# Optimization experiments

Hardware: AMD Instinct MI355X
Metric: run time of the kernel (lower is better)

## Reference

```python
import jax, jax.numpy as jnp
import numpy as np

B, C, H, W = 8, 256, 128, 128
WH, WW = 8, 8
M, NH = 4, 8
N = WH * WW
HD = C // NH
SCALE = HD ** -0.5


def _ln(x, g, b, eps=1e-5):
    m = x.mean(-1, keepdims=True)
    v = ((x - m) ** 2).mean(-1, keepdims=True)
    return (x - m) / jnp.sqrt(v + eps) * g + b


def _wpart(x):
    # (B, H, W, C) -> (B*nW, WH*WW, C)
    b, h, w, c = x.shape
    x = x.reshape(b, h // WH, WH, w // WW, WW, c).transpose(0, 1, 3, 2, 4, 5)
    return x.reshape(-1, N, c)


def _wrev(x, h, w):
    # (B*nW, WH*WW, C) -> (B, H, W, C)
    c = x.shape[-1]
    b = x.shape[0] // ((h // WH) * (w // WW))
    x = x.reshape(b, h // WH, w // WW, WH, WW, c).transpose(0, 1, 3, 2, 4, 5)
    return x.reshape(b, h, w, c)


def setup_inputs() -> dict:
    key = jax.random.key(0)
    ks = iter(jax.random.split(key, 16))

    def rn(shape, s=0.02):
        return jax.random.normal(next(ks), shape, jnp.float32) * s

    z = lambda *s: jnp.zeros(s, jnp.float32)
    o = lambda *s: jnp.ones(s, jnp.float32)
    return {
        'F_R': jax.random.normal(next(ks), (B, C, H, W), jnp.float32),
        'F_T': jax.random.normal(next(ks), (B, C, H, W), jnp.float32),
        'r_R': jax.random.uniform(next(ks), (B, 1, H, W), jnp.float32),
        'r_T': jax.random.uniform(next(ks), (B, 1, H, W), jnp.float32),
        'psi_w': rn((2 * C, M)), 'psi_b': z(M),
        'phi_w': rn((2 * C, 2 * C)), 'phi_b': z(2 * C),
        'np_g': o(2 * C), 'np_b': z(2 * C),
        'nz_g': o(C), 'nz_b': z(C),
        'rpb_table': rn(((2 * WH - 1) * (2 * WW - 1), NH)),
        'q_w': rn((C, C)), 'q_b': z(C),
        'k_w': rn((C, C)), 'k_b': z(C),
        'v_w': rn((C, C)), 'v_b': z(C),
        'nzf_g': o(C), 'nzf_b': z(C),
        'fc1_w': rn((C, 4 * C)), 'fc1_b': z(4 * C),
        'fc2_w': rn((4 * C, C)), 'fc2_b': z(C),
        'nr_g': o(C), 'nr_b': z(C),
        'nt_g': o(C), 'nt_b': z(C),
        'g1_w': rn((2, 8)), 'g1_b': z(8),
        'g2_w': rn((8, 1)), 'g2_b': z(1),
    }


def reference(F_R, F_T, r_R, r_T, psi_w, psi_b, phi_w, phi_b, np_g, np_b,
              nz_g, nz_b, rpb_table, q_w, q_b, k_w, k_b, v_w, v_b,
              nzf_g, nzf_b, fc1_w, fc1_b, fc2_w, fc2_b, nr_g, nr_b,
              nt_g, nt_b, g1_w, g1_b, g2_w, g2_b):
    # NOTE: rpb_table corresponds to relative_position_bias_table; the original
    # forward computes attn_mask = rel_pos_bias + local_mask but never applies it
    # (dead code), so it does not affect the output.
    FRw = _wpart(jnp.transpose(F_R, (0, 2, 3, 1)))  # (Bn, N, C)
    FTw = _wpart(jnp.transpose(F_T, (0, 2, 3, 1)))

    # attention pooling to mediators
    F_hat = _ln(jnp.concatenate([FRw, FTw], axis=-1), np_g, np_b)  # (Bn, N, 2C)
    A_m = jax.nn.softmax(F_hat @ psi_w + psi_b, axis=1)            # (Bn, N, M)
    Z = jnp.einsum('bnm,bnd->bmd', A_m, F_hat @ phi_w + phi_b)     # (Bn, M, 2C)
    Z = _ln((Z[..., :C] + Z[..., C:]) * 0.5, nz_g, nz_b)           # (Bn, M, C)

    rRw = _wpart(jnp.transpose(r_R, (0, 2, 3, 1)))[..., 0]  # (Bn, N)
    rTw = _wpart(jnp.transpose(r_T, (0, 2, 3, 1)))[..., 0]

    # mediators attend to each windowed stream
    QZ = (Z @ q_w + q_b).reshape(-1, M, NH, HD)
    KR = (FRw @ k_w + k_b).reshape(-1, N, NH, HD)
    VR = (FRw @ v_w + v_b).reshape(-1, N, NH, HD)
    KT = (FTw @ k_w + k_b).reshape(-1, N, NH, HD)
    VT = (FTw @ v_w + v_b).reshape(-1, N, NH, HD)

    aR = jax.nn.softmax(jnp.einsum('bmhd,bnhd->bhmn', QZ, KR) * SCALE
                        * rRw[:, None, None, :], axis=-1)
    ZhR = jnp.einsum('bhmn,bnhd->bmhd', aR, VR).reshape(-1, M, C)
    aT = jax.nn.softmax(jnp.einsum('bmhd,bnhd->bhmn', QZ, KT) * SCALE
                        * rTw[:, None, None, :], axis=-1)
    ZhT = jnp.einsum('bhmn,bnhd->bmhd', aT, VT).reshape(-1, M, C)

    Zp = _ln(Z + ZhR + ZhT, nzf_g, nzf_b)
    Zp = jax.nn.gelu(Zp @ fc1_w + fc1_b, approximate=False) @ fc2_w + fc2_b

    # windows attend back to mediators (note cross r usage, as in the original)
    QR = (FRw @ q_w + q_b).reshape(-1, N, NH, HD)
    QT = (FTw @ q_w + q_b).reshape(-1, N, NH, HD)
    KZ = (Zp @ k_w + k_b).reshape(-1, M, NH, HD)
    VZ = (Zp @ v_w + v_b).reshape(-1, M, NH, HD)

    aZR = jax.nn.softmax(jnp.einsum('bnhd,bmhd->bhnm', QR, KZ) * SCALE
                         * rTw[:, None, :, None], axis=-1)
    FRh = jnp.einsum('bhnm,bmhd->bnhd', aZR, VZ).reshape(-1, N, C)
    aZT = jax.nn.softmax(jnp.einsum('bnhd,bmhd->bhnm', QT, KZ) * SCALE
                         * rRw[:, None, :, None], axis=-1)
    FTh = jnp.einsum('bhnm,bmhd->bnhd', aZT, VZ).reshape(-1, N, C)

    FRp = jnp.transpose(_wrev(_ln(FRw + FRh, nr_g, nr_b), H, W), (0, 3, 1, 2))
    FTp = jnp.transpose(_wrev(_ln(FTw + FTh, nt_g, nt_b), H, W), (0, 3, 1, 2))

    # gating from globally pooled relevance maps
    g_in = jnp.concatenate([r_R.mean((2, 3)), r_T.mean((2, 3))], axis=1)  # (B,2)
    gamma = jax.nn.sigmoid(jax.nn.relu(g_in @ g1_w + g1_b) @ g2_w + g2_b)  # (B,1)
    gamma = gamma[:, :, None, None]
    return gamma * FRp + (1.0 - gamma) * FTp
```

## Files before the change

kernel.cpp:

```cpp
#include <hip/hip_runtime.h>
#include <math.h>

#define SCALE 0.17677669529663687f

#define OFF_FRW  0l
#define OFF_FTW  33554432l
#define OFF_RRW  67108864l
#define OFF_RTW  67239936l
#define OFF_G    67371008l
#define OFF_Z    71565312l
#define OFF_ZP   73662464l
#define OFF_ZP2  75759616l
#define OFF_QT   77856768l
#define OFF_KT   77922304l
#define OFF_VT   77987840l
#define OFF_F1T  78053376l
#define OFF_PHIT 78315520l
#define OFF_PHB  78446592l
#define OFF_GAM  78446848l

__device__ __forceinline__ float wsum64(float v){
  #pragma unroll
  for(int o=32;o>0;o>>=1) v+=__shfl_xor(v,o,64);
  return v;
}
__device__ __forceinline__ float wmax64(float v){
  #pragma unroll
  for(int o=32;o>0;o>>=1) v=fmaxf(v,__shfl_xor(v,o,64));
  return v;
}
__device__ __forceinline__ float blockSum256(float v, float* red, int t){
  v=wsum64(v);
  __syncthreads();
  if((t&63)==0) red[t>>6]=v;
  __syncthreads();
  return red[0]+red[1]+red[2]+red[3];
}

__global__ __launch_bounds__(256) void k_prep(const float* __restrict__ qw, const float* __restrict__ kw,
                       const float* __restrict__ vw, const float* __restrict__ fc1w,
                       const float* __restrict__ phiw, const float* __restrict__ phibv,
                       float* __restrict__ ws){
  long gid = (long)blockIdx.x*256 + threadIdx.x;
  if(gid < 262144){ long o=gid>>8, i=gid&255; ws[OFF_F1T+gid] = fc1w[i*1024+o]; return; }
  gid -= 262144;
  if(gid < 65536){ long o=gid>>8, i=gid&255; ws[OFF_QT+gid] = qw[i*256+o]; return; }
  gid -= 65536;
  if(gid < 65536){ long o=gid>>8, i=gid&255; ws[OFF_KT+gid] = kw[i*256+o]; return; }
  gid -= 65536;
  if(gid < 65536){ long o=gid>>8, i=gid&255; ws[OFF_VT+gid] = vw[i*256+o]; return; }
  gid -= 65536;
  if(gid < 131072){ long c=gid>>9, k=gid&511; ws[OFF_PHIT+gid] = 0.5f*(phiw[k*512+c] + phiw[k*512+c+256]); return; }
  gid -= 131072;
  if(gid < 256){ ws[OFF_PHB+gid] = 0.5f*(phibv[gid] + phibv[gid+256]); }
}

__global__ __launch_bounds__(256) void k_gamma(const float* __restrict__ rR, const float* __restrict__ rT,
                        const float* __restrict__ g1w, const float* __restrict__ g1b,
                        const float* __restrict__ g2w, const float* __restrict__ g2b,
                        float* __restrict__ ws){
// ... 40 lines not shown
    }
    __syncthreads();
    int cl=t&31, tg=t>>5;
    for(int tok=tg; tok<1024; tok+=8){
      int wc=tok>>6, n=tok&63, i=n>>3, j=n&7;
      float v = tile[cl*TSTRC + i*TSTRI + wc*8+j];
      long w = ((long)b*16+wr)*16+wc;
      dst[(w*64+n)*256 + cchunk*32 + cl] = v;
    }
  }
  if(cchunk==0){
    for(int q=0;q<2;q++){
      const float* src=q? rT:rR;
      float* dst=ws + (q? OFF_RTW:OFF_RRW);
      for(int tok=t; tok<1024; tok+=256){
        int wc=tok>>6, n=tok&63, i=n>>3, j=n&7;
        long w=((long)b*16+wr)*16+wc;
        dst[w*64+n] = src[((long)b*128 + wr*8+i)*128 + wc*8+j];
      }
    }
  }
}

#define FS 516
__global__ __launch_bounds__(512) void k_stage1(const float* __restrict__ psiw, const float* __restrict__ psib,
                         const float* __restrict__ npg, const float* __restrict__ npb,
                         float* __restrict__ ws){
  __shared__ float F[64*FS];
  __shared__ float psiT[2048];
  __shared__ float ng[512], nb[512];
  __shared__ float mu[64], rsd[64];
  __shared__ float Sp[2048];
  __shared__ float Sa[256];
  int w=blockIdx.x, t=threadIdx.x;
  const float* FRw = ws+OFF_FRW + (long)w*16384;
  const float* FTw = ws+OFF_FTW + (long)w*16384;
  for(int i4=t;i4<8192;i4+=512){
    int n=i4>>7, cq=i4&127; int c=cq*4;
    float4 v = (c<256)? *(const float4*)(FRw + n*256+c) : *(const float4*)(FTw + n*256+c-256);
    float* p=&F[n*FS+c]; p[0]=v.x; p[1]=v.y; p[2]=v.z; p[3]=v.w;
  }
  ng[t&511]=npg[t&511]; nb[t&511]=npb[t&511];
  for(int i=t;i<2048;i+=512){ int c=i>>2, m=i&3; psiT[m*512+c]=psiw[i]; }
  __syncthreads();
  { int g=t>>6, l=t&63;
    for(int n=g;n<64;n+=8){
      float s1=0.f,s2=0.f;
      #pragma unroll
      for(int k=0;k<8;k++){ float x=F[n*FS + l + 64*k]; s1+=x; s2+=x*x; }
      s1=wsum64(s1); s2=wsum64(s2);
      if(l==0){ float mm=s1*(1.f/512.f), vv=s2*(1.f/512.f)-mm*mm; mu[n]=mm; rsd[n]=rsqrtf(vv+1e-5f); }
    } }
  __syncthreads();
  for(int i=t;i<32768;i+=512){ int n=i>>9, c=i&511; F[n*FS+c] = (F[n*FS+c]-mu[n])*rsd[n]*ng[c]+nb[c]; }
  __syncthreads();
  { int n=t&63, sl=t>>6; int c0=sl*64;
    float a0=0.f,a1=0.f,a2=0.f,a3=0.f;
    for(int k=0;k<64;k+=4){
      int c=c0+k;
      float4 f=*(const float4*)&F[n*FS+c];
      float4 p0=*(const float4*)&psiT[c];
      float4 p1=*(const float4*)&psiT[512+c];
      float4 p2=*(const float4*)&psiT[1024+c];
      float4 p3=*(const float4*)&psiT[1536+c];
      a0+=f.x*p0.x+f.y*p0.y+f.z*p0.z+f.w*p0.w;
      a1+=f.x*p1.x+f.y*p1.y+f.z*p1.z+f.w*p1.w;
      a2+=f.x*p2.x+f.y*p2.y+f.z*p2.z+f.w*p2.w;
      a3+=f.x*p3.x+f.y*p3.y+f.z*p3.z+f.w*p3.w;
    }
    float4 sv; sv.x=a0; sv.y=a1; sv.z=a2; sv.w=a3;
    *(float4*)&Sp[(sl*64+n)*4]=sv;
  }
  __syncthreads();
  if(t<256){ int n=t>>2, m=t&3;
    float s=psib[m];
    for(int sl=0;sl<8;sl++) s+=Sp[(sl*64+n)*4+m];
    Sa[n*4+m]=s;
  }
  __syncthreads();
  if(t<64){
    #pragma unroll
    for(int m=0;m<4;m++){
      float v=Sa[t*4+m];
      float mx=wmax64(v);
      float e=expf(v-mx);
      float sm=wsum64(e);
      Sa[t*4+m]=e/sm;
    } }
  __syncthreads();
  { int c=t;
    float a0=0.f,a1=0.f,a2=0.f,a3=0.f;
    for(int n=0;n<64;n++){
      float f=F[n*FS+c];
      float4 am=*(const float4*)&Sa[n*4];
      a0+=am.x*f; a1+=am.y*f; a2+=am.z*f; a3+=am.w*f;
    }
    float* G=ws+OFF_G+(long)w*2048;
    G[c]=a0; G[512+c]=a1; G[1024+c]=a2; G[1536+c]=a3;
  }
}

__global__ __launch_bounds__(256) void k_z(const float* __restrict__ nzg, const float* __restrict__ nzb,
                    float* __restrict__ ws){
  __shared__ float Gw[2048];
  __shared__ float red[4];
  int w=blockIdx.x, t=threadIdx.x;
  const float* G=ws+OFF_G+(long)w*2048;
  for(int i4=t;i4<512;i4+=256){ *(float4*)&Gw[i4*4] = *(const float4*)&G[i4*4]; }
  __syncthreads();
  const float* phiT=ws+OFF_PHIT;
  const float* phb=ws+OFF_PHB;
  int c=t;
  float pb=phb[c];
  float a0=pb,a1=pb,a2=pb,a3=pb;
  const float* prow = phiT + (long)c*512;
  for(int k=0;k<512;k+=4){
// ... 1 lines not shown
    float4 g0=*(const float4*)&Gw[k];
    float4 g1=*(const float4*)&Gw[512+k];
    float4 g2=*(const float4*)&Gw[1024+k];
    float4 g3=*(const float4*)&Gw[1536+k];
    a0+=g0.x*pv.x+g0.y*pv.y+g0.z*pv.z+g0.w*pv.w;
    a1+=g1.x*pv.x+g1.y*pv.y+g1.z*pv.z+g1.w*pv.w;
    a2+=g2.x*pv.x+g2.y*pv.y+g2.z*pv.z+g2.w*pv.w;
    a3+=g3.x*pv.x+g3.y*pv.y+g3.z*pv.z+g3.w*pv.w;
  }
  float* Z=ws+OFF_Z+(long)w*1024;
  float g=nzg[c], b=nzb[c];
  float vals[4]={a0,a1,a2,a3};
  #pragma unroll
  for(int m=0;m<4;m++){
    float v=vals[m];
    float s1=blockSum256(v,red,t);
    float s2=blockSum256(v*v,red,t);
    float mm=s1*(1.f/256.f), vv=s2*(1.f/256.f)-mm*mm;
    float rs=rsqrtf(vv+1e-5f);
    Z[m*256+c]=(v-mm)*rs*g+b;
  }
}

#define FLS 260
__global__ __launch_bounds__(256) void k_attn1(const float* __restrict__ qb, const float* __restrict__ kw,
    const float* __restrict__ kb, const float* __restrict__ vb,
    const float* __restrict__ nzfg, const float* __restrict__ nzfb,
    float* __restrict__ ws){
  __shared__ float Fl[64*FLS];
  __shared__ float Qp[8192];
  __shared__ float Wl[8192];
  __shared__ float Zl[1024];
  __shared__ float QZ[1024];
  __shared__ float Al[2048];
  __shared__ float cbs[32];
  __shared__ float rl[64];
  __shared__ float red[4];
  int w=blockIdx.x, t=threadIdx.x;
  {
    const float* Z=ws+OFF_Z+(long)w*1024;
    for(int i=t;i<1024;i+=256) Zl[i]=Z[i];
  }
  __syncthreads();
  {
    const float* qrow=ws+OFF_QT+(long)t*256;
    float b0=qb[t];
    float a0=b0,a1=b0,a2=b0,a3=b0;
    for(int k=0;k<256;k+=4){
      float4 q4=*(const float4*)(qrow+k);
      float4 z0=*(const float4*)&Zl[k];
      float4 z1=*(const float4*)&Zl[256+k];
      float4 z2=*(const float4*)&Zl[512+k];
      float4 z3=*(const float4*)&Zl[768+k];
      a0+=z0.x*q4.x+z0.y*q4.y+z0.z*q4.z+z0.w*q4.w;
      a1+=z1.x*q4.x+z1.y*q4.y+z1.z*q4.z+z1.w*q4.w;
      a2+=z2.x*q4.x+z2.y*q4.y+z2.z*q4.z+z2.w*q4.w;
      a3+=z3.x*q4.x+z3.y*q4.y+z3.z*q4.z+z3.w*q4.w;
    }
    QZ[t]=a0; QZ[256+t]=a1; QZ[512+t]=a2; QZ[768+t]=a3;
  }
  __syncthreads();
  {
    const float* krow=kw+(long)t*256;
    for(int h=0;h<8;h++){
      float a0=0.f,a1=0.f,a2=0.f,a3=0.f;
      for(int d=0;d<32;d+=4){
        float4 k4=*(const float4*)(krow+h*32+d);
        float4 q0=*(const float4*)&QZ[h*32+d];
        float4 q1=*(const float4*)&QZ[256+h*32+d];
        float4 q2=*(const float4*)&QZ[512+h*32+d];
        float4 q3=*(const float4*)&QZ[768+h*32+d];
        a0+=k4.x*q0.x+k4.y*q0.y+k4.z*q0.z+k4.w*q0.w;
        a1+=k4.x*q1.x+k4.y*q1.y+k4.z*q1.z+k4.w*q1.w;
        a2+=k4.x*q2.x+k4.y*q2.y+k4.z*q2.z+k4.w*q2.w;
        a3+=k4.x*q3.x+k4.y*q3.y+k4.z*q3.z+k4.w*q3.w;
      }
      Qp[(h*4+0)*256+t]=a0; Qp[(h*4+1)*256+t]=a1; Qp[(h*4+2)*256+t]=a2; Qp[(h*4+3)*256+t]=a3;
    }
  }
  if(t<32){ int h=t>>2, m=t&3;
    float a=0.f;
    for(int d=0;d<32;d++) a+=kb[h*32+d]*QZ[m*256+h*32+d];
    cbs[t]=a;
  }
  for(int s=0;s<2;s++){
    __syncthreads();
    const float* Fsrc=ws+(s?OFF_FTW:OFF_FRW)+(long)w*16384;
    const float* rsrc=ws+(s?OFF_RTW:OFF_RRW)+(long)w*64;
    for(int i4=t;i4<4096;i4+=256){
      int n=i4>>6, cq=i4&63;
      float4 v=*(const float4*)(Fsrc+n*256+cq*4);
      float* p=&Fl[n*FLS+cq*4];
      p[0]=v.x; p[1]=v.y; p[2]=v.z; p[3]=v.w;
    }
    if(t<64) rl[t]=rsrc[t];
    __syncthreads();
    {
      int n=t&63, g=t>>6;
      const float* frow=&Fl[n*FLS];
      float acc[8];
      #pragma unroll
      for(int q=0;q<8;q++) acc[q]=cbs[q*4+g];
      for(int k=0;k<256;k+=4){
        float4 f=*(const float4*)(frow+k);
        #pragma unroll
        for(int q=0;q<8;q++){
          float4 p=*(const float4*)&Qp[(q*4+g)*256+k];
          acc[q]+=f.x*p.x+f.y*p.y+f.z*p.z+f.w*p.w;
        }
      }
      float sr=SCALE*rl[n];
      #pragma unroll
      for(int q=0;q<8;q++){
        float a=acc[q]*sr;
        float mx=wmax64(a);
        float e=expf(a-mx);
        float sm=wsum64(e);
        Al[(q*4+g)*64+n]=e/sm;
      }
    }
    __syncthreads();
    {
      int c=t;
      float wacc[32];
      #pragma unroll
      for(int P=0;P<32;P++) wacc[P]=0.f;
      for(int n0=0;n0<64;n0+=4){
        float f0=Fl[(n0+0)*FLS+c], f1=Fl[(n0+1)*FLS+c], f2=Fl[(n0+2)*FLS+c], f3=Fl[(n0+3)*FLS+c];
        #pragma unroll
        for(int P=0;P<32;P++){
          float4 a4=*(const float4*)&Al[P*64+n0];
          wacc[P]+=a4.x*f0+a4.y*f1+a4.z*f2+a4.w*f3;
        }
      }
      if(s==0){
        #pragma unroll
        for(int P=0;P<32;P++) Wl[P*256+c]=wacc[P];
      }else{
        #pragma unroll
        for(int P=0;P<32;P++) Wl[P*256+c]+=wacc[P];
      }
    }
  }
  __syncthreads();
  float zh0,zh1,zh2,zh3;
  {
    int co=t, h=co>>5;
    const float* vrow=ws+OFF_VT+(long)co*256;
    float vb2=2.f*vb[co];
    float a0=vb2,a1=vb2,a2=vb2,a3=vb2;
    for(int k=0;k<256;k+=4){
      float4 v4=*(const float4*)(vrow+k);
      float4 w0=*(const float4*)&Wl[(h*4+0)*256+k];
      float4 w1=*(const float4*)&Wl[(h*4+1)*256+k];
      float4 w2=*(const float4*)&Wl[(h*4+2)*256+k];
      float4 w3=*(const float4*)&Wl[(h*4+3)*256+k];
      a0+=w0.x*v4.x+w0.y*v4.y+w0.z*v4.z+w0.w*v4.w;
      a1+=w1.x*v4.x+w1.y*v4.y+w1.z*v4.z+w1.w*v4.w;
      a2+=w2.x*v4.x+w2.y*v4.y+w2.z*v4.z+w2.w*v4.w;
      a3+=w3.x*v4.x+w3.y*v4.y+w3.z*v4.z+w3.w*v4.w;
    }
    zh0=a0; zh1=a1; zh2=a2; zh3=a3;
  }
  {
    int c=t;
    float g=nzfg[c], b=nzfb[c];
    float* Zp=ws+OFF_ZP+(long)w*1024;
    float v4[4]={Zl[c]+zh0, Zl[256+c]+zh1, Zl[512+c]+zh2, Zl[768+c]+zh3};
    #pragma unroll
    for(int m=0;m<4;m++){
      float v=v4[m];
      float s1=blockSum256(v,red,t);
      float s2=blockSum256(v*v,red,t);
      float mm=s1*(1.f/256.f), vv=s2*(1.f/256.f)-mm*mm;
      float rs=rsqrtf(vv+1e-5f);
      Zp[m*256+c]=(v-mm)*rs*g+b;
    }
  }
}

__global__ __launch_bounds__(256) void k_mlp(const float* __restrict__ fc1b, const float* __restrict__ fc2w,
                      const float* __restrict__ fc2b, float* __restrict__ ws){
  __shared__ float Zpl[8192];
  __shared__ float Hc[4096];
  int blk=blockIdx.x, t=threadIdx.x;
  long r0=(long)blk*32;
  const float* Zp=ws+OFF_ZP + r0*256;
  for(int i4=t;i4<2048;i4+=256){ *(float4*)&Zpl[i4*4] = *(const float4*)&Zp[i4*4]; }
  float o[32];
  { float b=fc2b[t];
    #pragma unroll
    for(int r=0;r<32;r++) o[r]=b; }
  const float* f1T=ws+OFF_F1T;
  for(int ch=0;ch<8;ch++){
    __syncthreads();
    { int jl=t&127, rg=t>>7;
      int j=ch*128+jl;
      const float* wrow=f1T+(long)j*256;
      float acc[16];
      #pragma unroll
      for(int i=0;i<16;i++) acc[i]=0.f;
      for(int k=0;k<256;k+=4){
        float4 w4=*(const float4*)(wrow+k);
        #pragma unroll
        for(int i=0;i<16;i++){
          float4 z=*(const float4*)&Zpl[(rg*16+i)*256+k];
          acc[i]+=z.x*w4.x+z.y*w4.y+z.z*w4.z+z.w*w4.w;
        }
      }
      float bj=fc1b[j];
      #pragma unroll
      for(int i=0;i<16;i++){
        float x=acc[i]+bj;
        Hc[(rg*16+i)*128+jl]=0.5f*x*(1.f+erff(x*0.70710678118654752f));
      }
    }
    __syncthreads();
    { int c=t;
      const float* f2=fc2w+(long)(ch*128)*256+c;
      for(int j=0;j<128;j++){
        float wv=f2[(long)j*256];
        #pragma unroll
        for(int r=0;r<32;r++) o[r]+=Hc[r*128+j]*wv;
      }
    }
  }
  __syncthreads();
  float* Zp2=ws+OFF_ZP2 + r0*256;
  #pragma unroll
  for(int r=0;r<32;r++) Zp2[(long)r*256+t]=o[r];
}

__global__ __launch_bounds__(256) void k_final(const float* __restrict__ kbv, const float* __restrict__ qw,
    const float* __restrict__ qbv, const float* __restrict__ vbv,
    const float* __restrict__ nrg, const float* __restrict__ nrb,
    const float* __restrict__ ntg, const float* __restrict__ ntb,
    float* __restrict__ out, float* __restrict__ ws){
  __shared__ float Fl[64*FLS];
  __shared__ float Kp[8192];
  __shared__ float Z2[1024];
  __shared__ float KZ[1024];
  __shared__ float VZ[1024];
  __shared__ float Al[2048];
  __shared__ float cb2[32];
  __shared__ float rl[64];
  int w=blockIdx.x, t=threadIdx.x;
  int b=w>>8, wr=(w>>4)&15, wc=w&15;
  {
    const float* Zp2=ws+OFF_ZP2+(long)w*1024;
    for(int i=t;i<1024;i+=256) Z2[i]=Zp2[i];
  }
  __syncthreads();
  {
    const float* krow=ws+OFF_KT+(long)t*256;
    const float* vrow=ws+OFF_VT+(long)t*256;
    float kb0=kbv[t], vb0=vbv[t];
    float k0=kb0,k1=kb0,k2=kb0,k3=kb0, v0=vb0,v1=vb0,v2=vb0,v3=vb0;
    for(int k=0;k<256;k+=4){
      float4 kk=*(const float4*)(krow+k);
      float4 vv=*(const float4*)(vrow+k);
      float4 z0=*(const float4*)&Z2[k];
      float4 z1=*(const float4*)&Z2[256+k];
      float4 z2=*(const float4*)&Z2[512+k];
      float4 z3=*(const float4*)&Z2[768+k];
      k0+=z0.x*kk.x+z0.y*kk.y+z0.z*kk.z+z0.w*kk.w;
      k1+=z1.x*kk.x+z1.y*kk.y+z1.z*kk.z+z1.w*kk.w;
      k2+=z2.x*kk.x+z2.y*kk.y+z2.z*kk.z+z2.w*kk.w;
      k3+=z3.x*kk.x+z3.y*kk.y+z3.z*kk.z+z3.w*kk.w;
      v0+=z0.x*vv.x+z0.y*vv.y+z0.z*vv.z+z0.w*vv.w;
      v1+=z1.x*vv.x+z1.y*vv.y+z1.z*vv.z+z1.w*vv.w;
      v2+=z2.x*vv.x+z2.y*vv.y+z2.z*vv.z+z2.w*vv.w;
      v3+=z3.x*vv.x+z3.y*vv.y+z3.z*vv.z+z3.w*vv.w;
    }
    KZ[t]=k0; KZ[256+t]=k1; KZ[512+t]=k2; KZ[768+t]=k3;
    VZ[t]=v0; VZ[256+t]=v1; VZ[512+t]=v2; VZ[768+t]=v3;
  }
  __syncthreads();
  {
    const float* qrow=qw+(long)t*256;
    for(int h=0;h<8;h++){
      float a0=0.f,a1=0.f,a2=0.f,a3=0.f;
      for(int d=0;d<32;d+=4){
        float4 q4=*(const float4*)(qrow+h*32+d);
        float4 c0=*(const float4*)&KZ[h*32+d];
        float4 c1=*(const float4*)&KZ[256+h*32+d];
        float4 c2=*(const float4*)&KZ[512+h*32+d];
        float4 c3=*(const float4*)&KZ[768+h*32+d];
        a0+=q4.x*c0.x+q4.y*c0.y+q4.z*c0.z+q4.w*c0.w;
        a1+=q4.x*c1.x+q4.y*c1.y+q4.z*c1.z+q4.w*c1.w;
        a2+=q4.x*c2.x+q4.y*c2.y+q4.z*c2.z+q4.w*c2.w;
        a3+=q4.x*c3.x+q4.y*c3.y+q4.z*c3.z+q4.w*c3.w;
      }
      Kp[(h*4+0)*256+t]=a0; Kp[(h*4+1)*256+t]=a1; Kp[(h*4+2)*256+t]=a2; Kp[(h*4+3)*256+t]=a3;
    }
  }
  if(t<32){ int h=t>>2, m=t&3;
    float a=0.f;
    for(int d=0;d<32;d++) a+=qbv[h*32+d]*KZ[m*256+h*32+d];
    cb2[t]=a;
  }
  float gam=ws[OFF_GAM+b];
  float oa[64];
  int lane=t&63, wv=t>>6;
  for(int s=0;s<2;s++){
    __syncthreads();
    const float* Fsrc=ws+(s?OFF_FTW:OFF_FRW)+(long)w*16384;
    const float* rsrc=ws+(s?OFF_RRW:OFF_RTW)+(long)w*64;
    for(int i4=t;i4<4096;i4+=256){
      int n=i4>>6, cq=i4&63;
      float4 v=*(const float4*)(Fsrc+n*256+cq*4);
      float* p=&Fl[n*FLS+cq*4];
      p[0]=v.x; p[1]=v.y; p[2]=v.z; p[3]=v.w;
    }
    if(t<64) rl[t]=rsrc[t];
    __syncthreads();
    {
      int n=lane;
      const float* frow=&Fl[n*FLS];
      float sr=SCALE*rl[n];
      #pragma unroll
      for(int hh=0;hh<2;hh++){
        int h=wv*2+hh;
        float a0=cb2[h*4+0],a1=cb2[h*4+1],a2=cb2[h*4+2],a3=cb2[h*4+3];
        for(int k=0;k<256;k+=4){
          float4 f=*(const float4*)(frow+k);
          float4 p0=*(const float4*)&Kp[(h*4+0)*256+k];
          float4 p1=*(const float4*)&Kp[(h*4+1)*256+k];
          float4 p2=*(const float4*)&Kp[(h*4+2)*256+k];
          float4 p3=*(const float4*)&Kp[(h*4+3)*256+k];
          a0+=f.x*p0.x+f.y*p0.y+f.z*p0.z+f.w*p0.w;
          a1+=f.x*p1.x+f.y*p1.y+f.z*p1.z+f.w*p1.w;
          a2+=f.x*p2.x+f.y*p2.y+f.z*p2.z+f.w*p2.w;
          a3+=f.x*p3.x+f.y*p3.y+f.z*p3.z+f.w*p3.w;
        }
        a0*=sr; a1*=sr; a2*=sr; a3*=sr;
        float mx=fmaxf(fmaxf(a0,a1),fmaxf(a2,a3));
        float e0=expf(a0-mx),e1=expf(a1-mx),e2=expf(a2-mx),e3=expf(a3-mx);
        float inv=1.f/(e0+e1+e2+e3);
        float4 av; av.x=e0*inv; av.y=e1*inv; av.z=e2*inv; av.w=e3*inv;
        *(float4*)&Al[(h*64+n)*4]=av;
      }
    }
    __syncthreads();
    {
      float gsc = s? (1.f-gam) : gam;
      float vzr[4][4], gA[4], bA[4];
      #pragma unroll
      for(int e=0;e<4;e++){
        int c=lane+64*e;
        #pragma unroll
        for(int m=0;m<4;m++) vzr[e][m]=VZ[m*256+c];
        gA[e]= s? ntg[c]:nrg[c];
        bA[e]= s? ntb[c]:nrb[c];
      }
      for(int k=0;k<16;k++){
        int n=wv+4*k;
        float val[4]; float s1=0.f,s2=0.f;
        #pragma unroll
        for(int e=0;e<4;e++){
          int c=lane+64*e; int h=c>>5;
          float4 a4=*(const float4*)&Al[(h*64+n)*4];
          float v=Fl[n*FLS+c] + a4.x*vzr[e][0]+a4.y*vzr[e][1]+a4.z*vzr[e][2]+a4.w*vzr[e][3];
          val[e]=v; s1+=v; s2+=v*v;
        }
        s1=wsum64(s1); s2=wsum64(s2);
        float mm=s1*(1.f/256.f), vv2=s2*(1.f/256.f)-mm*mm;
        float rs=rsqrtf(vv2+1e-5f);
        #pragma unroll
        for(int e=0;e<4;e++){
          float lnv=(val[e]-mm)*rs*gA[e]+bA[e];
          if(s==0) oa[k*4+e]=gsc*lnv; else oa[k*4+e]+=gsc*lnv;
        }
      }
    }
  }
  __syncthreads();
  for(int k=0;k<16;k++){
    int n=wv+4*k;
    #pragma unroll
    for(int e=0;e<4;e++){ Fl[n*FLS+lane+64*e]=oa[k*4+e]; }
  }
  __syncthreads();
  {
    int c=t;
    long obase=((long)b*256+c)*16384 + (long)wr*1024 + wc*8;
    for(int i=0;i<8;i++){
      float4 v0, v1;
      v0.x=Fl[(i*8+0)*FLS+c]; v0.y=Fl[(i*8+1)*FLS+c]; v0.z=Fl[(i*8+2)*FLS+c]; v0.w=Fl[(i*8+3)*FLS+c];
      v1.x=Fl[(i*8+4)*FLS+c]; v1.y=Fl[(i*8+5)*FLS+c]; v1.z=Fl[(i*8+6)*FLS+c]; v1.w=Fl[(i*8+7)*FLS+c];
      *(float4*)(out+obase+(long)i*128)=v0;
      *(float4*)(out+obase+(long)i*128+4)=v1;
    }
  }
}

extern "C" void kernel_launch(void* const* d_in, const int* in_sizes, int n_in,
                              void* d_out, int out_size, void* d_ws, size_t ws_size,
                              hipStream_t stream){
  (void)in_sizes; (void)n_in; (void)out_size; (void)ws_size;
  const float* F_R=(const float*)d_in[0];
  const float* F_T=(const float*)d_in[1];
  const float* r_R=(const float*)d_in[2];
  const float* r_T=(const float*)d_in[3];
  const float* psi_w=(const float*)d_in[4];
  const float* psi_b=(const float*)d_in[5];
  const float* phi_w=(const float*)d_in[6];
  const float* phi_b=(const float*)d_in[7];
  const float* np_g=(const float*)d_in[8];
  const float* np_b=(const float*)d_in[9];
  const float* nz_g=(const float*)d_in[10];
  const float* nz_b=(const float*)d_in[11];
  const float* q_w=(const float*)d_in[13];
// ... 4 lines not shown
  const float* v_b=(const float*)d_in[18];
  const float* nzf_g=(const float*)d_in[19];
  const float* nzf_b=(const float*)d_in[20];
  const float* fc1_w=(const float*)d_in[21];
  const float* fc1_b=(const float*)d_in[22];
  const float* fc2_w=(const float*)d_in[23];
  const float* fc2_b=(const float*)d_in[24];
  const float* nr_g=(const float*)d_in[25];
  const float* nr_b=(const float*)d_in[26];
  const float* nt_g=(const float*)d_in[27];
  const float* nt_b=(const float*)d_in[28];
  const float* g1_w=(const float*)d_in[29];
  const float* g1_b=(const float*)d_in[30];
  const float* g2_w=(const float*)d_in[31];
  const float* g2_b=(const float*)d_in[32];
  float* ws=(float*)d_ws;
  float* out=(float*)d_out;

  hipLaunchKernelGGL(k_prep,  dim3(2305), dim3(256), 0, stream, q_w,k_w,v_w,fc1_w,phi_w,phi_b,ws);
  hipLaunchKernelGGL(k_gamma, dim3(8),    dim3(256), 0, stream, r_R,r_T,g1_w,g1_b,g2_w,g2_b,ws);
  hipLaunchKernelGGL(k_win,   dim3(8,16,8), dim3(256), 0, stream, F_R,F_T,r_R,r_T,ws);
  hipLaunchKernelGGL(k_stage1,dim3(2048), dim3(512), 0, stream, psi_w,psi_b,np_g,np_b,ws);
  hipLaunchKernelGGL(k_z,     dim3(2048), dim3(256), 0, stream, nz_g,nz_b,ws);
  hipLaunchKernelGGL(k_attn1, dim3(2048), dim3(256), 0, stream, q_b,k_w,k_b,v_b,nzf_g,nzf_b,ws);
  hipLaunchKernelGGL(k_mlp,   dim3(256),  dim3(256), 0, stream, fc1_b,fc2_w,fc2_b,ws);
  hipLaunchKernelGGL(k_final, dim3(2048), dim3(256), 0, stream, k_b,q_w,q_b,v_b,nr_g,nr_b,nt_g,nt_b,out,ws);
}
```

Measured before the change: 2.428 ms.

## Swizzle shared-memory layouts and double threads per block in attention kernels

Replaces padded shared-memory rows with an XOR swizzle in stage1, attn1 and final so the row and column reads avoid bank conflicts without padding. The attn1 and final kernels move from 256 to 512 threads: matvec reductions are split into two K-halves and summed through shared memory, and the per-head score and output work is split across the extra waves. The MLP kernel processes 16 rows per block instead of 32, doubling its grid. This aims to raise occupancy and latency hiding, at the cost of extra barriers and partial-sum passes, plus higher register and LDS pressure per block.

```diff
diff --git a/kernel.cpp b/kernel.cpp
--- a/kernel.cpp
+++ b/kernel.cpp
@@ -36,6 +36,18 @@
   __syncthreads();
   return red[0]+red[1]+red[2]+red[3];
 }
+__device__ __forceinline__ float blockSum512(float v, float* red, int t){
+  v=wsum64(v);
+  __syncthreads();
+  if((t&63)==0) red[t>>6]=v;
+  __syncthreads();
+  return red[0]+red[1]+red[2]+red[3]+red[4]+red[5]+red[6]+red[7];
+}
+
+__device__ __forceinline__ int swz(int n, int c){ return (n<<8) + ((((c>>2)^(n&15))<<2) | (c&3)); }
+__device__ __forceinline__ int swz4(int n, int c4){ return (n<<8) + ((c4^(n&15))<<2); }
+__device__ __forceinline__ int swz512(int n, int c){ return (n<<9) + ((((c>>2)^(n&15))<<2) | (c&3)); }
+__device__ __forceinline__ int swz512_4(int n, int c4){ return (n<<9) + ((c4^(n&15))<<2); }
 
 __global__ __launch_bounds__(256) void k_prep(const float* __restrict__ qw, const float* __restrict__ kw,
                        const float* __restrict__ vw, const float* __restrict__ fc1w,
@@ -122,11 +134,10 @@
   }
 }
 
-#define FS 516
 __global__ __launch_bounds__(512) void k_stage1(const float* __restrict__ psiw, const float* __restrict__ psib,
                          const float* __restrict__ npg, const float* __restrict__ npb,
                          float* __restrict__ ws){
-  __shared__ float F[64*FS];
+  __shared__ float F[64*512];
   __shared__ float psiT[2048];
   __shared__ float ng[512], nb[512];
   __shared__ float mu[64], rsd[64];
@@ -138,27 +149,27 @@
   for(int i4=t;i4<8192;i4+=512){
     int n=i4>>7, cq=i4&127; int c=cq*4;
     float4 v = (c<256)? *(const float4*)(FRw + n*256+c) : *(const float4*)(FTw + n*256+c-256);
-    float* p=&F[n*FS+c]; p[0]=v.x; p[1]=v.y; p[2]=v.z; p[3]=v.w;
-  }
-  ng[t&511]=npg[t&511]; nb[t&511]=npb[t&511];
+    *(float4*)&F[swz512_4(n,cq)] = v;
+  }
+  ng[t]=npg[t]; nb[t]=npb[t];
   for(int i=t;i<2048;i+=512){ int c=i>>2, m=i&3; psiT[m*512+c]=psiw[i]; }
   __syncthreads();
   { int g=t>>6, l=t&63;
     for(int n=g;n<64;n+=8){
       float s1=0.f,s2=0.f;
       #pragma unroll
-      for(int k=0;k<8;k++){ float x=F[n*FS + l + 64*k]; s1+=x; s2+=x*x; }
+      for(int k=0;k<8;k++){ float x=F[swz512(n, l+64*k)]; s1+=x; s2+=x*x; }
       s1=wsum64(s1); s2=wsum64(s2);
       if(l==0){ float mm=s1*(1.f/512.f), vv=s2*(1.f/512.f)-mm*mm; mu[n]=mm; rsd[n]=rsqrtf(vv+1e-5f); }
     } }
   __syncthreads();
-  for(int i=t;i<32768;i+=512){ int n=i>>9, c=i&511; F[n*FS+c] = (F[n*FS+c]-mu[n])*rsd[n]*ng[c]+nb[c]; }
-  __syncthreads();
-  { int n=t&63, sl=t>>6; int c0=sl*64;
+  for(int i=t;i<32768;i+=512){ int n=i>>9, c=i&511; int a=swz512(n,c); F[a] = (F[a]-mu[n])*rsd[n]*ng[c]+nb[c]; }
+  __syncthreads();
+  { int n=t&63, sl=t>>6; int c0=sl*64; int nx=n&15;
     float a0=0.f,a1=0.f,a2=0.f,a3=0.f;
     for(int k=0;k<64;k+=4){
-      int c=c0+k;
-      float4 f=*(const float4*)&F[n*FS+c];
+      int c=c0+k; int c4=c>>2;
+      float4 f=*(const float4*)&F[swz512_4(n,c4)];
       float4 p0=*(const float4*)&psiT[c];
       float4 p1=*(const float4*)&psiT[512+c];
       float4 p2=*(const float4*)&psiT[1024+c];
@@ -170,6 +181,7 @@
     }
     float4 sv; sv.x=a0; sv.y=a1; sv.z=a2; sv.w=a3;
     *(float4*)&Sp[(sl*64+n)*4]=sv;
+    (void)nx;
   }
   __syncthreads();
   if(t<256){ int n=t>>2, m=t&3;
@@ -191,7 +203,7 @@
   { int c=t;
     float a0=0.f,a1=0.f,a2=0.f,a3=0.f;
     for(int n=0;n<64;n++){
-      float f=F[n*FS+c];
+      float f=F[swz512(n,c)];
       float4 am=*(const float4*)&Sa[n*4];
       a0+=am.x*f; a1+=am.y*f; a2+=am.z*f; a3+=am.w*f;
     }
@@ -239,12 +251,11 @@
   }
 }
 
-#define FLS 260
-__global__ __launch_bounds__(256) void k_attn1(const float* __restrict__ qb, const float* __restrict__ kw,
+__global__ __launch_bounds__(512) void k_attn1(const float* __restrict__ qb, const float* __restrict__ kw,
     const float* __restrict__ kb, const float* __restrict__ vb,
     const float* __restrict__ nzfg, const float* __restrict__ nzfb,
     float* __restrict__ ws){
-  __shared__ float Fl[64*FLS];
+  __shared__ float Fl[16384];
   __shared__ float Qp[8192];
   __shared__ float Wl[8192];
   __shared__ float Zl[1024];
@@ -252,34 +263,45 @@
   __shared__ float Al[2048];
   __shared__ float cbs[32];
   __shared__ float rl[64];
-  __shared__ float red[4];
+  __shared__ float red[8];
   int w=blockIdx.x, t=threadIdx.x;
   {
     const float* Z=ws+OFF_Z+(long)w*1024;
-    for(int i=t;i<1024;i+=256) Zl[i]=Z[i];
-  }
-  __syncthreads();
-  {
-    const float* qrow=ws+OFF_QT+(long)t*256;
-    float b0=qb[t];
-    float a0=b0,a1=b0,a2=b0,a3=b0;
-    for(int k=0;k<256;k+=4){
+    for(int i=t;i<1024;i+=512) Zl[i]=Z[i];
+  }
+  __syncthreads();
+  {
+    int oo=t&255, half=t>>8; int kb0=half*128;
+    const float* qrow=ws+OFF_QT+(long)oo*256+kb0;
+    float a0=0.f,a1=0.f,a2=0.f,a3=0.f;
+    for(int k=0;k<128;k+=4){
       float4 q4=*(const float4*)(qrow+k);
-      float4 z0=*(const float4*)&Zl[k];
-      float4 z1=*(const float4*)&Zl[256+k];
-      float4 z2=*(const float4*)&Zl[512+k];
-      float4 z3=*(const float4*)&Zl[768+k];
+      float4 z0=*(const float4*)&Zl[kb0+k];
+      float4 z1=*(const float4*)&Zl[256+kb0+k];
+      float4 z2=*(const float4*)&Zl[512+kb0+k];
+      float4 z3=*(const float4*)&Zl[768+kb0+k];
       a0+=z0.x*q4.x+z0.y*q4.y+z0.z*q4.z+z0.w*q4.w;
       a1+=z1.x*q4.x+z1.y*q4.y+z1.z*q4.z+z1.w*q4.w;
       a2+=z2.x*q4.x+z2.y*q4.y+z2.z*q4.z+z2.w*q4.w;
       a3+=z3.x*q4.x+z3.y*q4.y+z3.z*q4.z+z3.w*q4.w;
     }
-    QZ[t]=a0; QZ[256+t]=a1; QZ[512+t]=a2; QZ[768+t]=a3;
-  }
-  __syncthreads();
-  {
-    const float* krow=kw+(long)t*256;
-    for(int h=0;h<8;h++){
+    int ab=half*1024+oo;
+    Al[ab]=a0; Al[ab+256]=a1; Al[ab+512]=a2; Al[ab+768]=a3;
+  }
+  __syncthreads();
+  if(t<256){
+    float b0=qb[t];
+    QZ[t]      =Al[t]     +Al[1024+t]+b0;
+    QZ[256+t]  =Al[256+t] +Al[1280+t]+b0;
+    QZ[512+t]  =Al[512+t] +Al[1536+t]+b0;
+    QZ[768+t]  =Al[768+t] +Al[1792+t]+b0;
+  }
+  __syncthreads();
+  {
+    int o=t&255, hb=(t>>8)*4;
+    const float* krow=kw+(long)o*256;
+    for(int hh=0;hh<4;hh++){
+      int h=hb+hh;
       float a0=0.f,a1=0.f,a2=0.f,a3=0.f;
       for(int d=0;d<32;d+=4){
         float4 k4=*(const float4*)(krow+h*32+d);
@@ -292,7 +314,7 @@
         a2+=k4.x*q2.x+k4.y*q2.y+k4.z*q2.z+k4.w*q2.w;
         a3+=k4.x*q3.x+k4.y*q3.y+k4.z*q3.z+k4.w*q3.w;
       }
-      Qp[(h*4+0)*256+t]=a0; Qp[(h*4+1)*256+t]=a1; Qp[(h*4+2)*256+t]=a2; Qp[(h*4+3)*256+t]=a3;
+      Qp[(h*4+0)*256+o]=a0; Qp[(h*4+1)*256+o]=a1; Qp[(h*4+2)*256+o]=a2; Qp[(h*4+3)*256+o]=a3;
     }
   }
   if(t<32){ int h=t>>2, m=t&3;
@@ -300,136 +322,142 @@
     for(int d=0;d<32;d++) a+=kb[h*32+d]*QZ[m*256+h*32+d];
     cbs[t]=a;
   }
+  int pc=t&255, ph=t>>8;
+  int sn=t&63, sh=t>>6, snx=sn&15;
+  float wacc[16];
+  #pragma unroll
+  for(int p=0;p<16;p++) wacc[p]=0.f;
   for(int s=0;s<2;s++){
     __syncthreads();
     const float* Fsrc=ws+(s?OFF_FTW:OFF_FRW)+(long)w*16384;
     const float* rsrc=ws+(s?OFF_RTW:OFF_RRW)+(long)w*64;
-    for(int i4=t;i4<4096;i4+=256){
-      int n=i4>>6, cq=i4&63;
-      float4 v=*(const float4*)(Fsrc+n*256+cq*4);
-      float* p=&Fl[n*FLS+cq*4];
-      p[0]=v.x; p[1]=v.y; p[2]=v.z; p[3]=v.w;
+    for(int i4=t;i4<4096;i4+=512){
+      int n=i4>>6, c4=i4&63;
+      *(float4*)&Fl[swz4(n,c4)] = *(const float4*)(Fsrc+n*256+c4*4);
     }
     if(t<64) rl[t]=rsrc[t];
     __syncthreads();
     {
-      int n=t&63, g=t>>6;
-      const float* frow=&Fl[n*FLS];
-      float acc[8];
+      const float* frow=&Fl[sn<<8];
+      float a0=cbs[sh*4+0],a1=cbs[sh*4+1],a2=cbs[sh*4+2],a3=cbs[sh*4+3];
+      for(int k4=0;k4<64;k4++){
+        float4 f=*(const float4*)(frow+((k4^snx)<<2));
+        int k=k4<<2;
+        float4 p0=*(const float4*)&Qp[(sh*4+0)*256+k];
+        float4 p1=*(const float4*)&Qp[(sh*4+1)*256+k];
+        float4 p2=*(const float4*)&Qp[(sh*4+2)*256+k];
+        float4 p3=*(const float4*)&Qp[(sh*4+3)*256+k];
+        a0+=f.x*p0.x+f.y*p0.y+f.z*p0.z+f.w*p0.w;
+        a1+=f.x*p1.x+f.y*p1.y+f.z*p1.z+f.w*p1.w;
+        a2+=f.x*p2.x+f.y*p2.y+f.z*p2.z+f.w*p2.w;
+        a3+=f.x*p3.x+f.y*p3.y+f.z*p3.z+f.w*p3.w;
+      }
+      float sr=SCALE*rl[sn];
+      float av[4]={a0,a1,a2,a3};
       #pragma unroll
-      for(int q=0;q<8;q++) acc[q]=cbs[q*4+g];
-      for(int k=0;k<256;k+=4){
-        float4 f=*(const float4*)(frow+k);
-        #pragma unroll
-        for(int q=0;q<8;q++){
-          float4 p=*(const float4*)&Qp[(q*4+g)*256+k];
-          acc[q]+=f.x*p.x+f.y*p.y+f.z*p.z+f.w*p.w;
-        }
-      }
-      float sr=SCALE*rl[n];
-      #pragma unroll
-      for(int q=0;q<8;q++){
-        float a=acc[q]*sr;
+      for(int m=0;m<4;m++){
+        float a=av[m]*sr;
         float mx=wmax64(a);
         float e=expf(a-mx);
         float sm=wsum64(e);
-        Al[(q*4+g)*64+n]=e/sm;
+        Al[(sh*4+m)*64+sn]=e/sm;
       }
     }
     __syncthreads();
     {
-      int c=t;
-      float wacc[32];
-      #pragma unroll
-      for(int P=0;P<32;P++) wacc[P]=0.f;
       for(int n0=0;n0<64;n0+=4){
-        float f0=Fl[(n0+0)*FLS+c], f1=Fl[(n0+1)*FLS+c], f2=Fl[(n0+2)*FLS+c], f3=Fl[(n0+3)*FLS+c];
+        float f0=Fl[swz(n0+0,pc)];
+        float f1=Fl[swz(n0+1,pc)];
+        float f2=Fl[swz(n0+2,pc)];
+        float f3=Fl[swz(n0+3,pc)];
         #pragma unroll
-        for(int P=0;P<32;P++){
-          float4 a4=*(const float4*)&Al[P*64+n0];
-          wacc[P]+=a4.x*f0+a4.y*f1+a4.z*f2+a4.w*f3;
+        for(int p=0;p<16;p++){
+          float4 a4=*(const float4*)&Al[(ph*16+p)*64+n0];
+          wacc[p]+=a4.x*f0+a4.y*f1+a4.z*f2+a4.w*f3;
         }
       }
-      if(s==0){
-        #pragma unroll
-        for(int P=0;P<32;P++) Wl[P*256+c]=wacc[P];
-      }else{
-        #pragma unroll
-        for(int P=0;P<32;P++) Wl[P*256+c]+=wacc[P];
-      }
-    }
-  }
-  __syncthreads();
-  float zh0,zh1,zh2,zh3;
-  {
-    int co=t, h=co>>5;
-    const float* vrow=ws+OFF_VT+(long)co*256;
-    float vb2=2.f*vb[co];
-    float a0=vb2,a1=vb2,a2=vb2,a3=vb2;
-    for(int k=0;k<256;k+=4){
+    }
+  }
+  #pragma unroll
+  for(int p=0;p<16;p++) Wl[(ph*16+p)*256+pc]=wacc[p];
+  __syncthreads();
+  {
+    int co=t&255, half=t>>8, h=co>>5; int kb0=half*128;
+    const float* vrow=ws+OFF_VT+(long)co*256+kb0;
+    float a0=0.f,a1=0.f,a2=0.f,a3=0.f;
+    for(int k=0;k<128;k+=4){
       float4 v4=*(const float4*)(vrow+k);
-      float4 w0=*(const float4*)&Wl[(h*4+0)*256+k];
-      float4 w1=*(const float4*)&Wl[(h*4+1)*256+k];
-      float4 w2=*(const float4*)&Wl[(h*4+2)*256+k];
-      float4 w3=*(const float4*)&Wl[(h*4+3)*256+k];
+      float4 w0=*(const float4*)&Wl[(h*4+0)*256+kb0+k];
+      float4 w1=*(const float4*)&Wl[(h*4+1)*256+kb0+k];
+      float4 w2=*(const float4*)&Wl[(h*4+2)*256+kb0+k];
+      float4 w3=*(const float4*)&Wl[(h*4+3)*256+kb0+k];
       a0+=w0.x*v4.x+w0.y*v4.y+w0.z*v4.z+w0.w*v4.w;
       a1+=w1.x*v4.x+w1.y*v4.y+w1.z*v4.z+w1.w*v4.w;
       a2+=w2.x*v4.x+w2.y*v4.y+w2.z*v4.z+w2.w*v4.w;
       a3+=w3.x*v4.x+w3.y*v4.y+w3.z*v4.z+w3.w*v4.w;
     }
-    zh0=a0; zh1=a1; zh2=a2; zh3=a3;
-  }
-  {
-    int c=t;
-    float g=nzfg[c], b=nzfb[c];
+    int ab=half*1024+co;
+    Al[ab]=a0; Al[ab+256]=a1; Al[ab+512]=a2; Al[ab+768]=a3;
+  }
+  __syncthreads();
+  {
+    float v4a[4]={0.f,0.f,0.f,0.f};
+    float g=0.f,bb=0.f;
+    if(t<256){
+      g=nzfg[t]; bb=nzfb[t];
+      float vb2=2.f*vb[t];
+      #pragma unroll
+      for(int m=0;m<4;m++) v4a[m]=Zl[m*256+t]+Al[m*256+t]+Al[1024+m*256+t]+vb2;
+    }
     float* Zp=ws+OFF_ZP+(long)w*1024;
-    float v4[4]={Zl[c]+zh0, Zl[256+c]+zh1, Zl[512+c]+zh2, Zl[768+c]+zh3};
     #pragma unroll
     for(int m=0;m<4;m++){
-      float v=v4[m];
-      float s1=blockSum256(v,red,t);
-      float s2=blockSum256(v*v,red,t);
-      float mm=s1*(1.f/256.f), vv=s2*(1.f/256.f)-mm*mm;
-      float rs=rsqrtf(vv+1e-5f);
-      Zp[m*256+c]=(v-mm)*rs*g+b;
+      float v=v4a[m];
+      float s1=blockSum512(v,red,t);
+      float s2=blockSum512(v*v,red,t);
+      if(t<256){
+        float mm=s1*(1.f/256.f), vv=s2*(1.f/256.f)-mm*mm;
+        float rs=rsqrtf(vv+1e-5f);
+        Zp[m*256+t]=(v-mm)*rs*g+bb;
+      }
     }
   }
 }
 
 __global__ __launch_bounds__(256) void k_mlp(const float* __restrict__ fc1b, const float* __restrict__ fc2w,
                       const float* __restrict__ fc2b, float* __restrict__ ws){
-  __shared__ float Zpl[8192];
-  __shared__ float Hc[4096];
+  __shared__ float Zpl[4096];
+  __shared__ float Hc[2048];
   int blk=blockIdx.x, t=threadIdx.x;
-  long r0=(long)blk*32;
+  long r0=(long)blk*16;
   const float* Zp=ws+OFF_ZP + r0*256;
-  for(int i4=t;i4<2048;i4+=256){ *(float4*)&Zpl[i4*4] = *(const float4*)&Zp[i4*4]; }
-  float o[32];
+  for(int i4=t;i4<1024;i4+=256){ *(float4*)&Zpl[i4*4] = *(const float4*)&Zp[i4*4]; }
+  float o[16];
   { float b=fc2b[t];
     #pragma unroll
-    for(int r=0;r<32;r++) o[r]=b; }
+    for(int r=0;r<16;r++) o[r]=b; }
   const float* f1T=ws+OFF_F1T;
   for(int ch=0;ch<8;ch++){
     __syncthreads();
     { int jl=t&127, rg=t>>7;
       int j=ch*128+jl;
       const float* wrow=f1T+(long)j*256;
-      float acc[16];
+      float acc[8];
       #pragma unroll
-      for(int i=0;i<16;i++) acc[i]=0.f;
+      for(int i=0;i<8;i++) acc[i]=0.f;
       for(int k=0;k<256;k+=4){
         float4 w4=*(const float4*)(wrow+k);
         #pragma unroll
-        for(int i=0;i<16;i++){
-          float4 z=*(const float4*)&Zpl[(rg*16+i)*256+k];
+        for(int i=0;i<8;i++){
+          float4 z=*(const float4*)&Zpl[(rg*8+i)*256+k];
           acc[i]+=z.x*w4.x+z.y*w4.y+z.z*w4.z+z.w*w4.w;
         }
       }
       float bj=fc1b[j];
       #pragma unroll
-      for(int i=0;i<16;i++){
+      for(int i=0;i<8;i++){
         float x=acc[i]+bj;
-        Hc[(rg*16+i)*128+jl]=0.5f*x*(1.f+erff(x*0.70710678118654752f));
+        Hc[(rg*8+i)*128+jl]=0.5f*x*(1.f+erff(x*0.70710678118654752f));
       }
     }
     __syncthreads();
@@ -438,22 +466,21 @@
       for(int j=0;j<128;j++){
         float wv=f2[(long)j*256];
         #pragma unroll
-        for(int r=0;r<32;r++) o[r]+=Hc[r*128+j]*wv;
-      }
-    }
-  }
-  __syncthreads();
+        for(int r=0;r<16;r++) o[r]+=Hc[r*128+j]*wv;
+      }
+    }
+  }
   float* Zp2=ws+OFF_ZP2 + r0*256;
   #pragma unroll
-  for(int r=0;r<32;r++) Zp2[(long)r*256+t]=o[r];
-}
-
-__global__ __launch_bounds__(256) void k_final(const float* __restrict__ kbv, const float* __restrict__ qw,
+  for(int r=0;r<16;r++) Zp2[(long)r*256+t]=o[r];
+}
+
+__global__ __launch_bounds__(512) void k_final(const float* __restrict__ kbv, const float* __restrict__ qw,
     const float* __restrict__ qbv, const float* __restrict__ vbv,
     const float* __restrict__ nrg, const float* __restrict__ nrb,
     const float* __restrict__ ntg, const float* __restrict__ ntb,
     float* __restrict__ out, float* __restrict__ ws){
-  __shared__ float Fl[64*FLS];
+  __shared__ float Fl[16384];
   __shared__ float Kp[8192];
   __shared__ float Z2[1024];
   __shared__ float KZ[1024];
@@ -465,21 +492,21 @@
   int b=w>>8, wr=(w>>4)&15, wc=w&15;
   {
     const float* Zp2=ws+OFF_ZP2+(long)w*1024;
-    for(int i=t;i<1024;i+=256) Z2[i]=Zp2[i];
-  }
-  __syncthreads();
-  {
-    const float* krow=ws+OFF_KT+(long)t*256;
-    const float* vrow=ws+OFF_VT+(long)t*256;
-    float kb0=kbv[t], vb0=vbv[t];
-    float k0=kb0,k1=kb0,k2=kb0,k3=kb0, v0=vb0,v1=vb0,v2=vb0,v3=vb0;
-    for(int k=0;k<256;k+=4){
+    for(int i=t;i<1024;i+=512) Z2[i]=Zp2[i];
+  }
+  __syncthreads();
+  {
+    int oo=t&255, half=t>>8; int kb0=half*128;
+    const float* krow=ws+OFF_KT+(long)oo*256+kb0;
+    const float* vrow=ws+OFF_VT+(long)oo*256+kb0;
+    float k0=0.f,k1=0.f,k2=0.f,k3=0.f, v0=0.f,v1=0.f,v2=0.f,v3=0.f;
+    for(int k=0;k<128;k+=4){
       float4 kk=*(const float4*)(krow+k);
       float4 vv=*(const float4*)(vrow+k);
-      float4 z0=*(const float4*)&Z2[k];
-      float4 z1=*(const float4*)&Z2[256+k];
-      float4 z2=*(const float4*)&Z2[512+k];
-      float4 z3=*(const float4*)&Z2[768+k];
+      float4 z0=*(const float4*)&Z2[kb0+k];
+      float4 z1=*(const float4*)&Z2[256+kb0+k];
+      float4 z2=*(const float4*)&Z2[512+kb0+k];
+      float4 z3=*(const float4*)&Z2[768+kb0+k];
       k0+=z0.x*kk.x+z0.y*kk.y+z0.z*kk.z+z0.w*kk.w;
       k1+=z1.x*kk.x+z1.y*kk.y+z1.z*kk.z+z1.w*kk.w;
       k2+=z2.x*kk.x+z2.y*kk.y+z2.z*kk.z+z2.w*kk.w;
@@ -489,13 +516,25 @@
       v2+=z2.x*vv.x+z2.y*vv.y+z2.z*vv.z+z2.w*vv.w;
       v3+=z3.x*vv.x+z3.y*vv.y+z3.z*vv.z+z3.w*vv.w;
     }
-    KZ[t]=k0; KZ[256+t]=k1; KZ[512+t]=k2; KZ[768+t]=k3;
-    VZ[t]=v0; VZ[256+t]=v1; VZ[512+t]=v2; VZ[768+t]=v3;
-  }
-  __syncthreads();
-  {
-    const float* qrow=qw+(long)t*256;
-    for(int h=0;h<8;h++){
+    int ab=half*1024+oo;
+    Kp[ab]=k0; Kp[ab+256]=k1; Kp[ab+512]=k2; Kp[ab+768]=k3;
+    Kp[4096+ab]=v0; Kp[4096+ab+256]=v1; Kp[4096+ab+512]=v2; Kp[4096+ab+768]=v3;
+  }
+  __syncthreads();
+  if(t<256){
+    float kb0=kbv[t], vb0=vbv[t];
+    #pragma unroll
+    for(int m=0;m<4;m++){
+      KZ[m*256+t]=Kp[m*256+t]+Kp[1024+m*256+t]+kb0;
+      VZ[m*256+t]=Kp[4096+m*256+t]+Kp[5120+m*256+t]+vb0;
+    }
+  }
+  __syncthreads();
+  {
+    int o=t&255, hb=(t>>8)*4;
+    const float* qrow=qw+(long)o*256;
+    for(int hh=0;hh<4;hh++){
+      int h=hb+hh;
       float a0=0.f,a1=0.f,a2=0.f,a3=0.f;
       for(int d=0;d<32;d+=4){
         float4 q4=*(const float4*)(qrow+h*32+d);
@@ -508,7 +547,7 @@
         a2+=q4.x*c2.x+q4.y*c2.y+q4.z*c2.z+q4.w*c2.w;
         a3+=q4.x*c3.x+q4.y*c3.y+q4.z*c3.z+q4.w*c3.w;
       }
-      Kp[(h*4+0)*256+t]=a0; Kp[(h*4+1)*256+t]=a1; Kp[(h*4+2)*256+t]=a2; Kp[(h*4+3)*256+t]=a3;
+      Kp[(h*4+0)*256+o]=a0; Kp[(h*4+1)*256+o]=a1; Kp[(h*4+2)*256+o]=a2; Kp[(h*4+3)*256+o]=a3;
     }
   }
   if(t<32){ int h=t>>2, m=t&3;
@@ -517,46 +556,41 @@
     cb2[t]=a;
   }
   float gam=ws[OFF_GAM+b];
-  float oa[64];
-  int lane=t&63, wv=t>>6;
+  float oa[32];
+  int lane=t&63, wv=t>>6, snx=lane&15;
   for(int s=0;s<2;s++){
     __syncthreads();
     const float* Fsrc=ws+(s?OFF_FTW:OFF_FRW)+(long)w*16384;
     const float* rsrc=ws+(s?OFF_RRW:OFF_RTW)+(long)w*64;
-    for(int i4=t;i4<4096;i4+=256){
-      int n=i4>>6, cq=i4&63;
-      float4 v=*(const float4*)(Fsrc+n*256+cq*4);
-      float* p=&Fl[n*FLS+cq*4];
-      p[0]=v.x; p[1]=v.y; p[2]=v.z; p[3]=v.w;
+    for(int i4=t;i4<4096;i4+=512){
+      int n=i4>>6, c4=i4&63;
+      *(float4*)&Fl[swz4(n,c4)] = *(const float4*)(Fsrc+n*256+c4*4);
     }
     if(t<64) rl[t]=rsrc[t];
     __syncthreads();
     {
-      int n=lane;
-      const float* frow=&Fl[n*FLS];
-      float sr=SCALE*rl[n];
-      #pragma unroll
-      for(int hh=0;hh<2;hh++){
-        int h=wv*2+hh;
-        float a0=cb2[h*4+0],a1=cb2[h*4+1],a2=cb2[h*4+2],a3=cb2[h*4+3];
-        for(int k=0;k<256;k+=4){
-          float4 f=*(const float4*)(frow+k);
-          float4 p0=*(const float4*)&Kp[(h*4+0)*256+k];
-          float4 p1=*(const float4*)&Kp[(h*4+1)*256+k];
-          float4 p2=*(const float4*)&Kp[(h*4+2)*256+k];
-          float4 p3=*(const float4*)&Kp[(h*4+3)*256+k];
-          a0+=f.x*p0.x+f.y*p0.y+f.z*p0.z+f.w*p0.w;
-          a1+=f.x*p1.x+f.y*p1.y+f.z*p1.z+f.w*p1.w;
-          a2+=f.x*p2.x+f.y*p2.y+f.z*p2.z+f.w*p2.w;
-          a3+=f.x*p3.x+f.y*p3.y+f.z*p3.z+f.w*p3.w;
-        }
-        a0*=sr; a1*=sr; a2*=sr; a3*=sr;
-        float mx=fmaxf(fmaxf(a0,a1),fmaxf(a2,a3));
-        float e0=expf(a0-mx),e1=expf(a1-mx),e2=expf(a2-mx),e3=expf(a3-mx);
-        float inv=1.f/(e0+e1+e2+e3);
-        float4 av; av.x=e0*inv; av.y=e1*inv; av.z=e2*inv; av.w=e3*inv;
-        *(float4*)&Al[(h*64+n)*4]=av;
-      }
+      const float* frow=&Fl[lane<<8];
+      int h=wv;
+      float a0=cb2[h*4+0],a1=cb2[h*4+1],a2=cb2[h*4+2],a3=cb2[h*4+3];
+      for(int k4=0;k4<64;k4++){
+        float4 f=*(const float4*)(frow+((k4^snx)<<2));
+        int k=k4<<2;
+        float4 p0=*(const float4*)&Kp[(h*4+0)*256+k];
+        float4 p1=*(const float4*)&Kp[(h*4+1)*256+k];
+        float4 p2=*(const float4*)&Kp[(h*4+2)*256+k];
+        float4 p3=*(const float4*)&Kp[(h*4+3)*256+k];
+        a0+=f.x*p0.x+f.y*p0.y+f.z*p0.z+f.w*p0.w;
+        a1+=f.x*p1.x+f.y*p1.y+f.z*p1.z+f.w*p1.w;
+        a2+=f.x*p2.x+f.y*p2.y+f.z*p2.z+f.w*p2.w;
+        a3+=f.x*p3.x+f.y*p3.y+f.z*p3.z+f.w*p3.w;
+      }
+      float sr=SCALE*rl[lane];
+      a0*=sr; a1*=sr; a2*=sr; a3*=sr;
+      float mx=fmaxf(fmaxf(a0,a1),fmaxf(a2,a3));
+      float e0=expf(a0-mx),e1=expf(a1-mx),e2=expf(a2-mx),e3=expf(a3-mx);
+      float inv=1.f/(e0+e1+e2+e3);
+      float4 av; av.x=e0*inv; av.y=e1*inv; av.z=e2*inv; av.w=e3*inv;
+      *(float4*)&Al[(h*64+lane)*4]=av;
     }
     __syncthreads();
     {
@@ -570,14 +604,14 @@
         gA[e]= s? ntg[c]:nrg[c];
         bA[e]= s? ntb[c]:nrb[c];
       }
-      for(int k=0;k<16;k++){
-        int n=wv+4*k;
+      for(int k=0;k<8;k++){
+        int n=wv+8*k;
         float val[4]; float s1=0.f,s2=0.f;
         #pragma unroll
         for(int e=0;e<4;e++){
-          int c=lane+64*e; int h=c>>5;
-          float4 a4=*(const float4*)&Al[(h*64+n)*4];
-          float v=Fl[n*FLS+c] + a4.x*vzr[e][0]+a4.y*vzr[e][1]+a4.z*vzr[e][2]+a4.w*vzr[e][3];
+          int c=lane+64*e; int h2=c>>5;
+          float4 a4=*(const float4*)&Al[(h2*64+n)*4];
+          float v=Fl[swz(n,c)] + a4.x*vzr[e][0]+a4.y*vzr[e][1]+a4.z*vzr[e][2]+a4.w*vzr[e][3];
           val[e]=v; s1+=v; s2+=v*v;
         }
         s1=wsum64(s1); s2=wsum64(s2);
@@ -592,19 +626,20 @@
     }
   }
   __syncthreads();
-  for(int k=0;k<16;k++){
-    int n=wv+4*k;
+  for(int k=0;k<8;k++){
+    int n=wv+8*k;
     #pragma unroll
-    for(int e=0;e<4;e++){ Fl[n*FLS+lane+64*e]=oa[k*4+e]; }
-  }
-  __syncthreads();
-  {
-    int c=t;
+    for(int e=0;e<4;e++){ Fl[swz(n,lane+64*e)]=oa[k*4+e]; }
+  }
+  __syncthreads();
+  {
+    int c=t&255, ih=t>>8;
     long obase=((long)b*256+c)*16384 + (long)wr*1024 + wc*8;
-    for(int i=0;i<8;i++){
+    for(int ii=0;ii<4;ii++){
+      int i=ih*4+ii;
       float4 v0, v1;
-      v0.x=Fl[(i*8+0)*FLS+c]; v0.y=Fl[(i*8+1)*FLS+c]; v0.z=Fl[(i*8+2)*FLS+c]; v0.w=Fl[(i*8+3)*FLS+c];
-      v1.x=Fl[(i*8+4)*FLS+c]; v1.y=Fl[(i*8+5)*FLS+c]; v1.z=Fl[(i*8+6)*FLS+c]; v1.w=Fl[(i*8+7)*FLS+c];
+      v0.x=Fl[swz(i*8+0,c)]; v0.y=Fl[swz(i*8+1,c)]; v0.z=Fl[swz(i*8+2,c)]; v0.w=Fl[swz(i*8+3,c)];
+      v1.x=Fl[swz(i*8+4,c)]; v1.y=Fl[swz(i*8+5,c)]; v1.z=Fl[swz(i*8+6,c)]; v1.w=Fl[swz(i*8+7,c)];
       *(float4*)(out+obase+(long)i*128)=v0;
       *(float4*)(out+obase+(long)i*128+4)=v1;
     }
@@ -655,7 +690,7 @@
   hipLaunchKernelGGL(k_win,   dim3(8,16,8), dim3(256), 0, stream, F_R,F_T,r_R,r_T,ws);
   hipLaunchKernelGGL(k_stage1,dim3(2048), dim3(512), 0, stream, psi_w,psi_b,np_g,np_b,ws);
   hipLaunchKernelGGL(k_z,     dim3(2048), dim3(256), 0, stream, nz_g,nz_b,ws);
-  hipLaunchKernelGGL(k_attn1, dim3(2048), dim3(256), 0, stream, q_b,k_w,k_b,v_b,nzf_g,nzf_b,ws);
-  hipLaunchKernelGGL(k_mlp,   dim3(256),  dim3(256), 0, stream, fc1_b,fc2_w,fc2_b,ws);
-  hipLaunchKernelGGL(k_final, dim3(2048), dim3(256), 0, stream, k_b,q_w,q_b,v_b,nr_g,nr_b,nt_g,nt_b,out,ws);
-}
+  hipLaunchKernelGGL(k_attn1, dim3(2048), dim3(512), 0, stream, q_b,k_w,k_b,v_b,nzf_g,nzf_b,ws);
+  hipLaunchKernelGGL(k_mlp,   dim3(512),  dim3(256), 0, stream, fc1_b,fc2_w,fc2_b,ws);
+  hipLaunchKernelGGL(k_final, dim3(2048), dim3(512), 0, stream, k_b,q_w,q_b,v_b,nr_g,nr_b,nt_g,nt_b,out,ws);
+}
```

Measured after the change: 2.326 ms. 1.04x faster.
